# Optimization experiments

Hardware: AMD Instinct MI355X
Metric: run time of the kernel (lower is better)

The kernel has to match this reference:

```python
import jax, jax.numpy as jnp
import numpy as np

EMBED_DIM = 1024
NUM_HEADS = 16
HEAD_DIM = EMBED_DIM // NUM_HEADS
B, S = 2, 2048


def setup_inputs() -> dict:
    key = jax.random.key(0)
    ks = jax.random.split(key, 9)
    scale = 1.0 / np.sqrt(EMBED_DIM)
    return {
        "x": jax.random.normal(ks[0], (B, S, EMBED_DIM), dtype=jnp.float32),
        "Wq": jax.random.normal(ks[1], (EMBED_DIM, EMBED_DIM), dtype=jnp.float32) * scale,
        "bq": jnp.zeros((EMBED_DIM,), dtype=jnp.float32),
        "Wk": jax.random.normal(ks[2], (EMBED_DIM, EMBED_DIM), dtype=jnp.float32) * scale,
        "bk": jnp.zeros((EMBED_DIM,), dtype=jnp.float32),
        "Wv": jax.random.normal(ks[3], (EMBED_DIM, EMBED_DIM), dtype=jnp.float32) * scale,
        "bv": jnp.zeros((EMBED_DIM,), dtype=jnp.float32),
        "Wo": jax.random.normal(ks[4], (EMBED_DIM, EMBED_DIM), dtype=jnp.float32) * scale,
        "bo": jnp.zeros((EMBED_DIM,), dtype=jnp.float32),
    }


def _split_heads(t):
    # [B, S, E] -> [B, H, S, Dh]
    b, s, _ = t.shape
    return t.reshape(b, s, NUM_HEADS, HEAD_DIM).transpose(0, 2, 1, 3)


def reference(x, Wq, bq, Wk, bk, Wv, bv, Wo, bo):
    q = _split_heads(x @ Wq + bq)
    k = _split_heads(x @ Wk + bk)
    v = _split_heads(x @ Wv + bv)
    scale = jnp.sqrt(jnp.asarray(HEAD_DIM, dtype=x.dtype))
    scores = jnp.einsum("bhqd,bhkd->bhqk", q, k) / scale
    attn = jax.nn.softmax(scores, axis=-1)
    out = jnp.einsum("bhqk,bhkd->bhqd", attn, v)  # [B,H,S,Dh]
    out = out.transpose(0, 2, 1, 3).reshape(x.shape[0], x.shape[1], EMBED_DIM)
    return out @ Wo + bo
```

## Files before the change

### kernel.cpp

```cpp
#include <hip/hip_runtime.h>
#include <math.h>
#include <stdint.h>

typedef __bf16 bf16;
typedef __bf16 bf16x4 __attribute__((ext_vector_type(4)));
typedef __bf16 bf16x8 __attribute__((ext_vector_type(8)));
typedef float f32x4 __attribute__((ext_vector_type(4)));
typedef float f32x16 __attribute__((ext_vector_type(16)));

constexpr int E = 1024;
constexpr int S = 2048;
constexpr int H = 16;

__device__ __forceinline__ void gload16(const void* g, void* l) {
  __builtin_amdgcn_global_load_lds(
      (__attribute__((address_space(1))) void*)(uintptr_t)g,
      (__attribute__((address_space(3))) void*)(uint32_t)(uintptr_t)l, 16, 0, 0);
}

__device__ __forceinline__ f32x4 mfma16(bf16x8 a, bf16x8 b, f32x4 c) {
  return __builtin_amdgcn_mfma_f32_16x16x32_bf16(a, b, c, 0, 0, 0);
}
__device__ __forceinline__ f32x16 mfma32(bf16x8 a, bf16x8 b, f32x16 c) {
  return __builtin_amdgcn_mfma_f32_32x32x16_bf16(a, b, c, 0, 0, 0);
}

__global__ __launch_bounds__(256) void cast_x(const float* __restrict__ x,
                                              bf16* __restrict__ o) {
  const size_t i = ((size_t)blockIdx.x * 256 + threadIdx.x) * 8;
  const float4 a = *(const float4*)(x + i);
  const float4 b = *(const float4*)(x + i + 4);
  bf16x8 r;
  r[0] = (bf16)a.x; r[1] = (bf16)a.y; r[2] = (bf16)a.z; r[3] = (bf16)a.w;
  r[4] = (bf16)b.x; r[5] = (bf16)b.y; r[6] = (bf16)b.z; r[7] = (bf16)b.w;
  *(bf16x8*)(o + i) = r;
}

__global__ __launch_bounds__(256) void transpose_cast_w(
    const float* __restrict__ W0, const float* __restrict__ W1,
    const float* __restrict__ W2, const float* __restrict__ W3,
    bf16* __restrict__ T0, bf16* __restrict__ T1, bf16* __restrict__ T2,
    bf16* __restrict__ T3) {
  const float* W;
  bf16* T;
  switch (blockIdx.z) {
    case 0: W = W0; T = T0; break;
    case 1: W = W1; T = T1; break;
    case 2: W = W2; T = T2; break;
    default: W = W3; T = T3; break;
  }
  __shared__ float t[64][65];
  const int k0 = blockIdx.y * 64, n0 = blockIdx.x * 64;
  const int tr = threadIdx.x >> 4;
  const int tc = (threadIdx.x & 15) * 4;
#pragma unroll
  for (int u = 0; u < 4; ++u) {
    const float4 v = *(const float4*)(W + (size_t)(k0 + tr + u * 16) * E + n0 + tc);
    t[tr + u * 16][tc + 0] = v.x;
    t[tr + u * 16][tc + 1] = v.y;
    t[tr + u * 16][tc + 2] = v.z;
    t[tr + u * 16][tc + 3] = v.w;
  }
  __syncthreads();
#pragma unroll
  for (int u = 0; u < 4; ++u) {
    const int n = tr + u * 16;
    bf16x4 o;
#pragma unroll
    for (int i = 0; i < 4; ++i) o[i] = (bf16)t[tc + i][n];
    *(bf16x4*)(T + (size_t)(n0 + n) * E + k0 + tc) = o;
  }
}

__global__ __launch_bounds__(256) void gemm_qkv(const bf16* __restrict__ A,
                                                const bf16* __restrict__ Wt,
                                                const float* __restrict__ bq,
                                                const float* __restrict__ bk,
                                                const float* __restrict__ bv,
                                                bf16* __restrict__ qo,
                                                bf16* __restrict__ ko,
                                                bf16* __restrict__ vo) {
  __shared__ __attribute__((aligned(16))) bf16 Asm[128 * 32];
  __shared__ __attribute__((aligned(16))) bf16 Bsm[128 * 32];
  const int z = blockIdx.z;
  const bf16* Bt = Wt + (size_t)z * E * E;
  const float* bias = (z == 0) ? bq : (z == 1) ? bk : bv;
  const int tid = threadIdx.x;
  const int w = tid >> 6, lane = tid & 63, quad = lane >> 4, ln = lane & 15;
  const int bm = blockIdx.y * 128, bn = blockIdx.x * 128;
  const int wr = w >> 1, wc = w & 1;
  const int srow = w * 32 + (lane >> 2);
  const int scol = (lane & 3) * 8;
  const bf16* Ag = A + (size_t)(bm + srow) * E + scol;
  const bf16* Bg = Bt + (size_t)(bn + srow) * E + scol;
  f32x4 acc[4][4] = {};

  for (int k0 = 0; k0 < E; k0 += 32) {
    gload16(Ag + k0, &Asm[(w * 32) * 32]);
    gload16(Ag + k0 + (size_t)16 * E, &Asm[(w * 32 + 16) * 32]);
    gload16(Bg + k0, &Bsm[(w * 32) * 32]);
    gload16(Bg + k0 + (size_t)16 * E, &Bsm[(w * 32 + 16) * 32]);
    __syncthreads();
    bf16x8 af[4], bfr[4];
#pragma unroll
    for (int t = 0; t < 4; ++t) {
      af[t] = *(const bf16x8*)&Asm[(wr * 64 + t * 16 + ln) * 32 + quad * 8];
      bfr[t] = *(const bf16x8*)&Bsm[(wc * 64 + t * 16 + ln) * 32 + quad * 8];
    }
#pragma unroll
    for (int rt = 0; rt < 4; ++rt)
#pragma unroll
      for (int ct = 0; ct < 4; ++ct)
        acc[rt][ct] = mfma16(af[rt], bfr[ct], acc[rt][ct]);
    __syncthreads();
  }

  const float scl = (z == 0) ? 0.125f : 1.0f;
  float bvv[4];
#pragma unroll
  for (int ct = 0; ct < 4; ++ct) bvv[ct] = bias[bn + wc * 64 + ct * 16 + ln];
#pragma unroll
  for (int rt = 0; rt < 4; ++rt) {
    const int row0 = bm + wr * 64 + rt * 16 + quad * 4;
#pragma unroll
    for (int ct = 0; ct < 4; ++ct) {
      const int c = bn + wc * 64 + ct * 16 + ln;
      if (z == 2) {
        bf16x4 p;
#pragma unroll
        for (int r = 0; r < 4; ++r) p[r] = (bf16)(acc[rt][ct][r] + bvv[ct]);
        const int bb = row0 >> 11;
        const int sin = row0 & 2047;
        *(bf16x4*)&vo[((size_t)(bb << 10) + c) * S + sin] = p;
      } else {
        bf16* o = (z == 0) ? qo : ko;
#pragma unroll
        for (int r = 0; r < 4; ++r)
          o[(size_t)(row0 + r) * E + c] = (bf16)((acc[rt][ct][r] + bvv[ct]) * scl);
      }
    }
  }
}

__global__ __launch_bounds__(256) void gemm_wo(const bf16* __restrict__ A,
                                               const bf16* __restrict__ Bt,
                                               const float* __restrict__ bias,
                                               float* __restrict__ C) {
  __shared__ __attribute__((aligned(16))) bf16 Asm[64 * 32];
  __shared__ __attribute__((aligned(16))) bf16 Bsm[128 * 32];
  const int tid = threadIdx.x;
  const int w = tid >> 6, lane = tid & 63, quad = lane >> 4, ln = lane & 15;
  const int bm = blockIdx.y * 64, bn = blockIdx.x * 128;
  const int wr = w >> 1, wc = w & 1;
  const int sr = lane >> 2, sc = (lane & 3) * 8;
  const bf16* Ag = A + (size_t)(bm + w * 16 + sr) * E + sc;
  const bf16* Bg = Bt + (size_t)(bn + w * 32 + sr) * E + sc;
  f32x4 acc[2][4] = {};

  for (int k0 = 0; k0 < E; k0 += 32) {
    gload16(Ag + k0, &Asm[(w * 16) * 32]);
    gload16(Bg + k0, &Bsm[(w * 32) * 32]);
    gload16(Bg + k0 + (size_t)16 * E, &Bsm[(w * 32 + 16) * 32]);
    __syncthreads();
    bf16x8 af[2], bfr[4];
#pragma unroll
    for (int t = 0; t < 2; ++t)
      af[t] = *(const bf16x8*)&Asm[(wr * 32 + t * 16 + ln) * 32 + quad * 8];
#pragma unroll
    for (int t = 0; t < 4; ++t)
      bfr[t] = *(const bf16x8*)&Bsm[(wc * 64 + t * 16 + ln) * 32 + quad * 8];
#pragma unroll
    for (int rt = 0; rt < 2; ++rt)
#pragma unroll
      for (int ct = 0; ct < 4; ++ct)
        acc[rt][ct] = mfma16(af[rt], bfr[ct], acc[rt][ct]);
    __syncthreads();
  }

  float bvv[4];
#pragma unroll
  for (int ct = 0; ct < 4; ++ct) bvv[ct] = bias[bn + wc * 64 + ct * 16 + ln];
#pragma unroll
  for (int rt = 0; rt < 2; ++rt) {
    const int row0 = bm + wr * 32 + rt * 16 + quad * 4;
#pragma unroll
    for (int ct = 0; ct < 4; ++ct) {
      const int c = bn + wc * 64 + ct * 16 + ln;
#pragma unroll
      for (int r = 0; r < 4; ++r)
        C[(size_t)(row0 + r) * E + c] = acc[rt][ct][r] + bvv[ct];
    }
  }
}

__global__ __launch_bounds__(256) void attn_mfma(const bf16* __restrict__ Qg,
                                                 const bf16* __restrict__ Kg,
                                                 const bf16* __restrict__ Vt,
                                                 bf16* __restrict__ Og) {
  __shared__ __attribute__((aligned(16))) bf16 Ks[2][64][72];
  __shared__ __attribute__((aligned(16))) bf16 Vs[2][64][72];
  __shared__ __attribute__((aligned(16))) bf16 Pl[4][32][72];
  const int tid = threadIdx.x;
  const int w = tid >> 6, lane = tid & 63, ln = lane & 31, hf = lane >> 5;
  const int q0 = blockIdx.x * 128, h = blockIdx.y, b = blockIdx.z;
  const size_t qkb = ((size_t)b * S) * E + (size_t)h * 64;
  const size_t vtb = ((size_t)b * E + (size_t)h * 64) * S;
  const int sr = tid >> 2;
  const int sc = (tid & 3) * 16;

  bf16x8 qf[4];
  {
    const bf16* qrow = Qg + qkb + (size_t)(q0 + w * 32 + ln) * E + hf * 8;
#pragma unroll
    for (int c = 0; c < 4; ++c) qf[c] = *(const bf16x8*)(qrow + 16 * c);
  }

  const bf16* Kp = Kg + qkb + (size_t)sr * E + sc;
  const bf16* Vp = Vt + vtb + (size_t)sr * S + sc;

  bf16x8 kr[2], vr[2];
  kr[0] = *(const bf16x8*)(Kp);
  kr[1] = *(const bf16x8*)(Kp + 8);
  vr[0] = *(const bf16x8*)(Vp);
  vr[1] = *(const bf16x8*)(Vp + 8);
  *(bf16x8*)&Ks[0][sr][sc] = kr[0];
  *(bf16x8*)&Ks[0][sr][sc + 8] = kr[1];
  *(bf16x8*)&Vs[0][sr][sc] = vr[0];
  *(bf16x8*)&Vs[0][sr][sc + 8] = vr[1];

  float lpart = 0.f;
  f32x16 oacc[2] = {};
  int cur = 0;

  for (int kt = 0; kt < S; kt += 64) {
    __syncthreads();
    const bool more = (kt + 64 < S);
    if (more) {
      kr[0] = *(const bf16x8*)(Kp + (size_t)(kt + 64) * E);
      kr[1] = *(const bf16x8*)(Kp + (size_t)(kt + 64) * E + 8);
      vr[0] = *(const bf16x8*)(Vp + (kt + 64));
      vr[1] = *(const bf16x8*)(Vp + (kt + 64) + 8);
    }

    f32x16 st[2] = {};
#pragma unroll
    for (int mt = 0; mt < 2; ++mt) {
#pragma unroll
      for (int c = 0; c < 4; ++c) {
        const bf16x8 ka =
            *(const bf16x8*)&Ks[cur][mt * 32 + ln][c * 16 + hf * 8];
        st[mt] = mfma32(ka, qf[c], st[mt]);
      }
    }

#pragma unroll
    for (int mt = 0; mt < 2; ++mt) {
#pragma unroll
      for (int g = 0; g < 4; ++g) {
        bf16x4 pk;
#pragma unroll
        for (int j = 0; j < 4; ++j) {
          const float p = __expf(st[mt][g * 4 + j]);
          lpart += p;
          pk[j] = (bf16)p;
        }
        *(bf16x4*)&Pl[w][ln][mt * 32 + g * 8 + hf * 4] = pk;
      }
    }
    asm volatile("s_waitcnt lgkmcnt(0)" ::: "memory");

    bf16x8 pb[4];
#pragma unroll
    for (int c = 0; c < 4; ++c)
      pb[c] = *(const bf16x8*)&Pl[w][ln][c * 16 + hf * 8];
#pragma unroll
    for (int mt = 0; mt < 2; ++mt) {
#pragma unroll
      for (int c = 0; c < 4; ++c) {
        const bf16x8 va =
            *(const bf16x8*)&Vs[cur][mt * 32 + ln][c * 16 + hf * 8];
        oacc[mt] = mfma32(va, pb[c], oacc[mt]);
      }
    }

    if (more) {
      *(bf16x8*)&Ks[cur ^ 1][sr][sc] = kr[0];
      *(bf16x8*)&Ks[cur ^ 1][sr][sc + 8] = kr[1];
      *(bf16x8*)&Vs[cur ^ 1][sr][sc] = vr[0];
      *(bf16x8*)&Vs[cur ^ 1][sr][sc + 8] = vr[1];
    }
    cur ^= 1;
  }

  lpart += __shfl_xor(lpart, 32);
  const float inv = 1.0f / lpart;

  bf16* orow = Og + qkb + (size_t)(q0 + w * 32 + ln) * E;
#pragma unroll
  for (int mt = 0; mt < 2; ++mt) {
#pragma unroll
    for (int g = 0; g < 4; ++g) {
      bf16x4 o;
#pragma unroll
      for (int j = 0; j < 4; ++j) o[j] = (bf16)(oacc[mt][g * 4 + j] * inv);
      *(bf16x4*)&orow[mt * 32 + g * 8 + hf * 4] = o;
    }
  }
}

extern "C" void kernel_launch(void* const* d_in, const int* in_sizes, int n_in,
                              void* d_out, int out_size, void* d_ws, size_t ws_size,
                              hipStream_t stream) {
  const float* x = (const float*)d_in[0];
  const float* Wq = (const float*)d_in[1];
  const float* bq = (const float*)d_in[2];
  const float* Wk = (const float*)d_in[3];
  const float* bk = (const float*)d_in[4];
  const float* Wv = (const float*)d_in[5];
  const float* bv = (const float*)d_in[6];
  const float* Wo = (const float*)d_in[7];
  const float* bo = (const float*)d_in[8];

  const size_t ME = (size_t)4096 * 1024;
  const size_t WE = (size_t)1024 * 1024;
  bf16* xb = (bf16*)d_ws;
  bf16* wqt = xb + ME;
  bf16* wkt = wqt + WE;
  bf16* wvt = wkt + WE;
  bf16* wot = wvt + WE;
  bf16* qb = wot + WE;
  bf16* kb = qb + ME;
  bf16* vt = kb + ME;
  bf16* ab = vt + ME;

  cast_x<<<2048, 256, 0, stream>>>(x, xb);
  transpose_cast_w<<<dim3(16, 16, 4), 256, 0, stream>>>(Wq, Wk, Wv, Wo, wqt, wkt,
                                                        wvt, wot);
  gemm_qkv<<<dim3(8, 32, 3), 256, 0, stream>>>(xb, wqt, bq, bk, bv, qb, kb, vt);
  attn_mfma<<<dim3(16, 16, 2), 256, 0, stream>>>(qb, kb, vt, ab);
  gemm_wo<<<dim3(8, 64), 256, 0, stream>>>(ab, wot, bo, (float*)d_out);
}
```

Measured before the change: 202.6 us.

## Store Q/K/V in MFMA-fragment order and load attention operands directly from global

```diff
diff --git a/kernel.cpp b/kernel.cpp
--- a/kernel.cpp
+++ b/kernel.cpp
@@ -11,6 +11,7 @@
 constexpr int E = 1024;
 constexpr int S = 2048;
 constexpr int H = 16;
+
 
 __device__ __forceinline__ void gload16(const void* g, void* l) {
   __builtin_amdgcn_global_load_lds(
@@ -116,27 +117,35 @@
   }
 
   const float scl = (z == 0) ? 0.125f : 1.0f;
+  const int hglob = (bn + wc * 64) >> 6;
   float bvv[4];
 #pragma unroll
   for (int ct = 0; ct < 4; ++ct) bvv[ct] = bias[bn + wc * 64 + ct * 16 + ln];
+
 #pragma unroll
   for (int rt = 0; rt < 4; ++rt) {
     const int row0 = bm + wr * 64 + rt * 16 + quad * 4;
+    const int bb = row0 >> 11;
+    const int rl = row0 & 2047;
+    const size_t hb = (size_t)(bb * 16 + hglob) * 131072;
 #pragma unroll
     for (int ct = 0; ct < 4; ++ct) {
-      const int c = bn + wc * 64 + ct * 16 + ln;
       if (z == 2) {
+        const int mt = ct >> 1, ln32 = ((ct & 1) << 4) | ln;
+        const int tau = rl >> 6, hfv = (rl >> 3) & 1, j0 = rl & 7;
         bf16x4 p;
 #pragma unroll
         for (int r = 0; r < 4; ++r) p[r] = (bf16)(acc[rt][ct][r] + bvv[ct]);
-        const int bb = row0 >> 11;
-        const int sin = row0 & 2047;
-        *(bf16x4*)&vo[((size_t)(bb << 10) + c) * S + sin] = p;
+        *(bf16x4*)&vo[hb + (size_t)((tau * 8 + mt * 4 + rt) * 512 +
+                                    hfv * 256 + ln32 * 8 + j0)] = p;
       } else {
         bf16* o = (z == 0) ? qo : ko;
+        const int t = rl >> 5, ln0 = rl & 31;
+        const size_t base =
+            hb + (size_t)((t * 4 + ct) * 512 + (ln >> 3) * 256 + (ln & 7));
 #pragma unroll
         for (int r = 0; r < 4; ++r)
-          o[(size_t)(row0 + r) * E + c] = (bf16)((acc[rt][ct][r] + bvv[ct]) * scl);
+          o[base + (ln0 + r) * 8] = (bf16)((acc[rt][ct][r] + bvv[ct]) * scl);
       }
     }
   }
@@ -193,64 +202,50 @@
   }
 }
 
-__global__ __launch_bounds__(256) void attn_mfma(const bf16* __restrict__ Qg,
-                                                 const bf16* __restrict__ Kg,
-                                                 const bf16* __restrict__ Vt,
-                                                 bf16* __restrict__ Og) {
-  __shared__ __attribute__((aligned(16))) bf16 Ks[2][64][72];
-  __shared__ __attribute__((aligned(16))) bf16 Vs[2][64][72];
-  __shared__ __attribute__((aligned(16))) bf16 Pl[4][32][72];
-  const int tid = threadIdx.x;
-  const int w = tid >> 6, lane = tid & 63, ln = lane & 31, hf = lane >> 5;
-  const int q0 = blockIdx.x * 128, h = blockIdx.y, b = blockIdx.z;
-  const size_t qkb = ((size_t)b * S) * E + (size_t)h * 64;
-  const size_t vtb = ((size_t)b * E + (size_t)h * 64) * S;
-  const int sr = tid >> 2;
-  const int sc = (tid & 3) * 16;
+__global__ __launch_bounds__(64) void attn_mfma(const bf16* __restrict__ Qf,
+                                                const bf16* __restrict__ Kf,
+                                                const bf16* __restrict__ Vf,
+                                                bf16* __restrict__ Og) {
+  __shared__ __attribute__((aligned(16))) bf16 Pl[32][74];
+  const int lane = threadIdx.x;
+  const int ln = lane & 31, hf = lane >> 5;
+  const int tq = blockIdx.x, h = blockIdx.y, b = blockIdx.z;
+  const int bh = b * H + h;
+  const size_t fb = (size_t)bh * 131072;
 
   bf16x8 qf[4];
   {
-    const bf16* qrow = Qg + qkb + (size_t)(q0 + w * 32 + ln) * E + hf * 8;
-#pragma unroll
-    for (int c = 0; c < 4; ++c) qf[c] = *(const bf16x8*)(qrow + 16 * c);
-  }
-
-  const bf16* Kp = Kg + qkb + (size_t)sr * E + sc;
-  const bf16* Vp = Vt + vtb + (size_t)sr * S + sc;
-
-  bf16x8 kr[2], vr[2];
-  kr[0] = *(const bf16x8*)(Kp);
-  kr[1] = *(const bf16x8*)(Kp + 8);
-  vr[0] = *(const bf16x8*)(Vp);
-  vr[1] = *(const bf16x8*)(Vp + 8);
-  *(bf16x8*)&Ks[0][sr][sc] = kr[0];
-  *(bf16x8*)&Ks[0][sr][sc + 8] = kr[1];
-  *(bf16x8*)&Vs[0][sr][sc] = vr[0];
-  *(bf16x8*)&Vs[0][sr][sc + 8] = vr[1];
+    const bf16* qb = Qf + fb + (size_t)tq * 2048 + lane * 8;
+#pragma unroll
+    for (int c = 0; c < 4; ++c) qf[c] = *(const bf16x8*)(qb + c * 512);
+  }
+
+  const bf16* Kb = Kf + fb + lane * 8;
+  const bf16* Vb = Vf + fb + lane * 8;
 
   float lpart = 0.f;
   f32x16 oacc[2] = {};
-  int cur = 0;
-
-  for (int kt = 0; kt < S; kt += 64) {
-    __syncthreads();
-    const bool more = (kt + 64 < S);
-    if (more) {
-      kr[0] = *(const bf16x8*)(Kp + (size_t)(kt + 64) * E);
-      kr[1] = *(const bf16x8*)(Kp + (size_t)(kt + 64) * E + 8);
-      vr[0] = *(const bf16x8*)(Vp + (kt + 64));
-      vr[1] = *(const bf16x8*)(Vp + (kt + 64) + 8);
-    }
-
-    f32x16 st[2] = {};
+
+  for (int kt2 = 0; kt2 < S / 32; kt2 += 2) {
+    f32x16 st[2];
 #pragma unroll
     for (int mt = 0; mt < 2; ++mt) {
-#pragma unroll
-      for (int c = 0; c < 4; ++c) {
-        const bf16x8 ka =
-            *(const bf16x8*)&Ks[cur][mt * 32 + ln][c * 16 + hf * 8];
-        st[mt] = mfma32(ka, qf[c], st[mt]);
-      }
+      const bf16* kb2 = Kb + (size_t)(kt2 + mt) * 2048;
+      f32x16 zz = {};
+#pragma unroll
+      for (int c = 0; c < 4; ++c)
+        zz = mfma32(*(const bf16x8*)(kb2 + c * 512), qf[c], zz);
+      st[mt] = zz;
+    }
+
+    bf16x8 va[2][4];
+    {
+      const bf16* vb2 = Vb + (size_t)(kt2 >> 1) * 4096;
+#pragma unroll
+      for (int mt = 0; mt < 2; ++mt)
+#pragma unroll
+        for (int c = 0; c < 4; ++c)
+          va[mt][c] = *(const bf16x8*)(vb2 + (mt * 4 + c) * 512);
     }
 
 #pragma unroll
@@ -264,7 +259,7 @@
           lpart += p;
           pk[j] = (bf16)p;
         }
-        *(bf16x4*)&Pl[w][ln][mt * 32 + g * 8 + hf * 4] = pk;
+        *(bf16x4*)&Pl[ln][mt * 32 + g * 8 + hf * 4] = pk;
       }
     }
     asm volatile("s_waitcnt lgkmcnt(0)" ::: "memory");
@@ -272,30 +267,18 @@
     bf16x8 pb[4];
 #pragma unroll
     for (int c = 0; c < 4; ++c)
-      pb[c] = *(const bf16x8*)&Pl[w][ln][c * 16 + hf * 8];
-#pragma unroll
-    for (int mt = 0; mt < 2; ++mt) {
-#pragma unroll
-      for (int c = 0; c < 4; ++c) {
-        const bf16x8 va =
-            *(const bf16x8*)&Vs[cur][mt * 32 + ln][c * 16 + hf * 8];
-        oacc[mt] = mfma32(va, pb[c], oacc[mt]);
-      }
-    }
-
-    if (more) {
-      *(bf16x8*)&Ks[cur ^ 1][sr][sc] = kr[0];
-      *(bf16x8*)&Ks[cur ^ 1][sr][sc + 8] = kr[1];
-      *(bf16x8*)&Vs[cur ^ 1][sr][sc] = vr[0];
-      *(bf16x8*)&Vs[cur ^ 1][sr][sc + 8] = vr[1];
-    }
-    cur ^= 1;
+      pb[c] = *(const bf16x8*)&Pl[ln][c * 16 + hf * 8];
+#pragma unroll
+    for (int mt = 0; mt < 2; ++mt)
+#pragma unroll
+      for (int c = 0; c < 4; ++c)
+        oacc[mt] = mfma32(va[mt][c], pb[c], oacc[mt]);
   }
 
   lpart += __shfl_xor(lpart, 32);
   const float inv = 1.0f / lpart;
 
-  bf16* orow = Og + qkb + (size_t)(q0 + w * 32 + ln) * E;
+  bf16* orow = Og + ((size_t)b * S + (size_t)tq * 32 + ln) * E + h * 64;
 #pragma unroll
   for (int mt = 0; mt < 2; ++mt) {
 #pragma unroll
@@ -337,6 +320,6 @@
   transpose_cast_w<<<dim3(16, 16, 4), 256, 0, stream>>>(Wq, Wk, Wv, Wo, wqt, wkt,
                                                         wvt, wot);
   gemm_qkv<<<dim3(8, 32, 3), 256, 0, stream>>>(xb, wqt, bq, bk, bv, qb, kb, vt);
-  attn_mfma<<<dim3(16, 16, 2), 256, 0, stream>>>(qb, kb, vt, ab);
+  attn_mfma<<<dim3(S / 32, H, 2), 64, 0, stream>>>(qb, kb, vt, ab);
   gemm_wo<<<dim3(8, 64), 256, 0, stream>>>(ab, wot, bo, (float*)d_out);
 }
```

New measurement: 204.2 us. About the same (+0.8%).
